# Kernel tuning notes

Hardware: AMD Instinct MI355X
Metric: run time of the kernel (lower is better)

Reference implementation:

```python
import jax, jax.numpy as jnp
import numpy as np


def setup_inputs() -> dict:
    key = jax.random.key(0)
    k1, k2 = jax.random.split(key)
    STATE_LEN, SEQ_LEN, HIDDEN = 8192, 8192, 1024
    out_state = jax.random.normal(k1, (STATE_LEN, HIDDEN), dtype=jnp.float32)
    history = jax.random.normal(k2, (SEQ_LEN, HIDDEN), dtype=jnp.float32)
    return {"out_state": out_state, "history": history}


def reference(out_state, history):
    # attn_energies[i, j] = dot(out_state[i], history[j])  ->  single GEMM
    energies = jnp.einsum('ih,jh->ij', out_state, history)  # [state_len, seq_len]
    # legacy F.softmax on a 2D tensor normalizes along dim=1 (the seq_len axis)
    return jax.nn.softmax(energies, axis=-1)
```

## Files before the change

### kernel.cpp

```cpp
#include <hip/hip_runtime.h>
#include <hip/hip_bf16.h>

#define M 8192
#define N 8192
#define K 1024
#define BM 128
#define BN 128
#define BK 64
#define ARR (BM*BK)

typedef __attribute__((ext_vector_type(8))) short short8;
typedef __attribute__((ext_vector_type(4))) float f32x4;

__device__ inline short f2bf(float x){
    __hip_bfloat16 h = __float2bfloat16(x);
    short s; __builtin_memcpy(&s, &h, 2); return s;
}
__device__ inline float bf2f(short s){
    __hip_bfloat16 h; __builtin_memcpy(&h, &s, 2);
    return __bfloat162float(h);
}

__device__ inline void conv8(float4 x0, float4 x1, short8& hi, short8& lo){
    float xs[8] = {x0.x,x0.y,x0.z,x0.w,x1.x,x1.y,x1.z,x1.w};
    #pragma unroll
    for (int j=0;j<8;++j){
        short h = f2bf(xs[j]);
        float r = xs[j] - bf2f(h);
        hi[j] = h; lo[j] = f2bf(r);
    }
}

__global__ __launch_bounds__(256) void presplit(
    const float* __restrict__ A, const float* __restrict__ B,
    short* __restrict__ Ah, short* __restrict__ Al,
    short* __restrict__ Bh, short* __restrict__ Bl)
{
    size_t c = (size_t)blockIdx.x * 256 + threadIdx.x;
    const float* src; short *dh, *dl; size_t off;
    const size_t perMat = (size_t)M * K / 8;
    if (c < perMat){ src = A; dh = Ah; dl = Al; off = c * 8; }
    else           { src = B; dh = Bh; dl = Bl; off = (c - perMat) * 8; }
    float4 x0 = *(const float4*)(src + off);
    float4 x1 = *(const float4*)(src + off + 4);
    short8 hi, lo;
    conv8(x0, x1, hi, lo);
    *(short8*)(dh + off) = hi;
    *(short8*)(dl + off) = lo;
}

#define GLOAD_LDS16(gp, lp) \
    __builtin_amdgcn_global_load_lds((const __attribute__((address_space(1))) void*)(gp), \
                                     (__attribute__((address_space(3))) void*)(lp), 16, 0, 0)

__global__ __launch_bounds__(512, 2)
void gemm_db(const short* __restrict__ Ahg, const short* __restrict__ Alg,
             const short* __restrict__ Bhg, const short* __restrict__ Blg,
             float* __restrict__ C)
{
    __shared__ __align__(16) short lds[2][4][ARR];

    const int tid  = threadIdx.x;
    const int lane = tid & 63, wid = tid >> 6;

    const int hw  = blockIdx.x;
    const int xcd = hw & 7;
    const int ix  = hw >> 3;
    const int gst = xcd * 32 + (ix >> 4);
    const int pos = ix & 15;
    const int bm0 = ((gst >> 4) * 4 + (pos >> 2)) * BM;
    const int bn0 = ((gst & 15) * 4 + (pos & 3)) * BN;

    const int wr = wid >> 2, wc = wid & 3;
    const int fr = lane & 15, fg = lane >> 4;

    f32x4 acc[4][2] = {};

    auto STAGE = [&](int buf, int kt){
        #pragma unroll
        for (int i = 0; i < 2; ++i){
            int bs = wid * 128 + i * 64;
            int s  = bs + lane;
            int row = s >> 3, sp = s & 7;
            int col8 = sp ^ (row & 7);
            size_t ga = (size_t)(bm0 + row) * K + kt * BK + col8 * 8;
            size_t gb = (size_t)(bn0 + row) * K + kt * BK + col8 * 8;
            GLOAD_LDS16(Ahg + ga, &lds[buf][0][bs * 8]);
            GLOAD_LDS16(Alg + ga, &lds[buf][1][bs * 8]);
            GLOAD_LDS16(Bhg + gb, &lds[buf][2][bs * 8]);
            GLOAD_LDS16(Blg + gb, &lds[buf][3][bs * 8]);
        }
    };

    STAGE(0, 0);
    __syncthreads();
    int cur = 0;

    for (int kt = 0; kt < K/BK; ++kt){
        if (kt + 1 < K/BK) STAGE(cur ^ 1, kt + 1);

        const short* sAh = lds[cur][0];
        const short* sAl = lds[cur][1];
        const short* sBh = lds[cur][2];
        const short* sBl = lds[cur][3];

        #pragma unroll
        for (int ks = 0; ks < 2; ++ks){
            short8 ah[4], al[4], bh[2], bl[2];
            #pragma unroll
            for (int m = 0; m < 4; ++m){
                int row = wr * 64 + m * 16 + fr;
                int idx = row * BK + ((((ks << 2) | fg) ^ (row & 7)) << 3);
                ah[m] = *(const short8*)&sAh[idx];
                al[m] = *(const short8*)&sAl[idx];
            }
            #pragma unroll
            for (int n = 0; n < 2; ++n){
                int row = wc * 32 + n * 16 + fr;
                int idx = row * BK + ((((ks << 2) | fg) ^ (row & 7)) << 3);
                bh[n] = *(const short8*)&sBh[idx];
                bl[n] = *(const short8*)&sBl[idx];
            }
            __builtin_amdgcn_s_setprio(1);
            #pragma unroll
            for (int m = 0; m < 4; ++m){
                #pragma unroll
                for (int n = 0; n < 2; ++n){
                    acc[m][n] = __builtin_amdgcn_mfma_f32_16x16x32_bf16(ah[m], bh[n], acc[m][n], 0, 0, 0);
                    acc[m][n] = __builtin_amdgcn_mfma_f32_16x16x32_bf16(ah[m], bl[n], acc[m][n], 0, 0, 0);
                    acc[m][n] = __builtin_amdgcn_mfma_f32_16x16x32_bf16(al[m], bh[n], acc[m][n], 0, 0, 0);
                }
            }
            __builtin_amdgcn_s_setprio(0);
        }
        __syncthreads();
        cur ^= 1;
    }

    #pragma unroll
    for (int m = 0; m < 4; ++m){
        int grow = bm0 + wr * 64 + m * 16 + fg * 4;
        #pragma unroll
        for (int r = 0; r < 4; ++r){
            float* crow = C + (size_t)(grow + r) * N + bn0 + wc * 32 + fr;
            crow[0]  = acc[m][0][r];
            crow[16] = acc[m][1][r];
        }
    }
}

__global__ __launch_bounds__(256, 2)
void gemm_fb(const float* __restrict__ A, const float* __restrict__ B,
             float* __restrict__ C)
{
    __shared__ __align__(16) short sAh[ARR];
    __shared__ __align__(16) short sAl[ARR];
    __shared__ __align__(16) short sBh[ARR];
    __shared__ __align__(16) short sBl[ARR];

    const int tid  = threadIdx.x;
    const int lane = tid & 63, wid = tid >> 6;
    const int bm0 = blockIdx.y * BM, bn0 = blockIdx.x * BN;
    const int wr = wid >> 1, wc = wid & 1;
    const int fr = lane & 15, fg = lane >> 4;

    f32x4 acc[4][4] = {};

    for (int kt = 0; kt < K/BK; ++kt){
        #pragma unroll
        for (int i = 0; i < 4; ++i){
            int s = tid + i * 256;
            int row = s >> 3, sp = s & 7;
            int widx = row * BK + ((sp ^ (row & 7)) << 3);
            const float* ga = A + (size_t)(bm0 + row) * K + kt * BK + sp * 8;
            float4 a0 = *(const float4*)ga, a1 = *(const float4*)(ga + 4);
            short8 hi, lo;
            conv8(a0, a1, hi, lo);
            *(short8*)&sAh[widx] = hi;
            *(short8*)&sAl[widx] = lo;
            const float* gb = B + (size_t)(bn0 + row) * K + kt * BK + sp * 8;
            float4 b0 = *(const float4*)gb, b1 = *(const float4*)(gb + 4);
            conv8(b0, b1, hi, lo);
            *(short8*)&sBh[widx] = hi;
            *(short8*)&sBl[widx] = lo;
        }
        __syncthreads();

        #pragma unroll
        for (int ks = 0; ks < 2; ++ks){
            short8 ah[4], al[4], bh[4], bl[4];
            #pragma unroll
            for (int m = 0; m < 4; ++m){
                int row = wr * 64 + m * 16 + fr;
                int idx = row * BK + ((((ks << 2) | fg) ^ (row & 7)) << 3);
                ah[m] = *(const short8*)&sAh[idx];
                al[m] = *(const short8*)&sAl[idx];
            }
            #pragma unroll
            for (int n = 0; n < 4; ++n){
                int row = wc * 64 + n * 16 + fr;
                int idx = row * BK + ((((ks << 2) | fg) ^ (row & 7)) << 3);
                bh[n] = *(const short8*)&sBh[idx];
                bl[n] = *(const short8*)&sBl[idx];
            }
            #pragma unroll
            for (int m = 0; m < 4; ++m){
                #pragma unroll
                for (int n = 0; n < 4; ++n){
                    acc[m][n] = __builtin_amdgcn_mfma_f32_16x16x32_bf16(ah[m], bh[n], acc[m][n], 0, 0, 0);
                    acc[m][n] = __builtin_amdgcn_mfma_f32_16x16x32_bf16(ah[m], bl[n], acc[m][n], 0, 0, 0);
                    acc[m][n] = __builtin_amdgcn_mfma_f32_16x16x32_bf16(al[m], bh[n], acc[m][n], 0, 0, 0);
                }
            }
        }
        __syncthreads();
    }

    #pragma unroll
    for (int m = 0; m < 4; ++m){
        int grow = bm0 + wr * 64 + m * 16 + fg * 4;
        #pragma unroll
        for (int r = 0; r < 4; ++r){
            float* crow = C + (size_t)(grow + r) * N + bn0 + wc * 64 + fr;
            #pragma unroll
            for (int n = 0; n < 4; ++n)
                crow[n * 16] = acc[m][n][r];
        }
    }
}

__global__ __launch_bounds__(256) void softmax_fused(float* __restrict__ E)
{
    const int row = blockIdx.x;
    const int tid = threadIdx.x;
    const int lane = tid & 63, wid = tid >> 6;
    float4* rp = (float4*)(E + (size_t)row * N);
    float4 v[8];
    float mx = -3.4e38f;
    #pragma unroll
    for (int i = 0; i < 8; ++i){
        v[i] = rp[tid + i * 256];
        mx = fmaxf(mx, fmaxf(fmaxf(v[i].x, v[i].y), fmaxf(v[i].z, v[i].w)));
    }
    #pragma unroll
    for (int off = 32; off; off >>= 1) mx = fmaxf(mx, __shfl_xor(mx, off));
    __shared__ float redm[4], reds[4];
    if (lane == 0) redm[wid] = mx;
    __syncthreads();
    mx = fmaxf(fmaxf(redm[0], redm[1]), fmaxf(redm[2], redm[3]));
    float s = 0.f;
    #pragma unroll
    for (int i = 0; i < 8; ++i){
        v[i].x = __expf(v[i].x - mx); v[i].y = __expf(v[i].y - mx);
        v[i].z = __expf(v[i].z - mx); v[i].w = __expf(v[i].w - mx);
        s += v[i].x + v[i].y + v[i].z + v[i].w;
    }
    #pragma unroll
    for (int off = 32; off; off >>= 1) s += __shfl_xor(s, off);
    if (lane == 0) reds[wid] = s;
    __syncthreads();
    float inv = 1.0f / (reds[0] + reds[1] + reds[2] + reds[3]);
    #pragma unroll
    for (int i = 0; i < 8; ++i){
        float4 o = v[i];
        o.x *= inv; o.y *= inv; o.z *= inv; o.w *= inv;
        rp[tid + i * 256] = o;
    }
}

extern "C" void kernel_launch(void* const* d_in, const int* in_sizes, int n_in,
                              void* d_out, int out_size, void* d_ws, size_t ws_size,
                              hipStream_t stream)
{
    const float* A = (const float*)d_in[0];
    const float* B = (const float*)d_in[1];
    float* out = (float*)d_out;

    const size_t elems = (size_t)M * K;
    const size_t splitBytes = 4 * elems * sizeof(short);

    if (ws_size >= splitBytes){
        short* Ah = (short*)d_ws;
        short* Al = Ah + elems;
        short* Bh = Al + elems;
        short* Bl = Bh + elems;
        presplit<<<8192, 256, 0, stream>>>(A, B, Ah, Al, Bh, Bl);
        gemm_db<<<(M/BM)*(N/BN), 512, 0, stream>>>(Ah, Al, Bh, Bl, out);
    } else {
        gemm_fb<<<dim3(N/BN, M/BM), 256, 0, stream>>>(A, B, out);
    }
    softmax_fused<<<M, 256, 0, stream>>>(out);
}
```

Measured before the change: 466.3 us.

## Use 256x256 tiles with k-major presplit layout for contiguous LDS loads

The presplit kernel now writes the bf16 hi/lo splits in a k8-major layout, so each 8-element k chunk for consecutive rows is contiguous. The GEMM tile grows from 128x128 to 256x256 with BK=32, and each wave owns an 8x4 grid of MFMA fragments. Each wave loads one array slice straight into LDS without swizzling, and the XCD-aware block remap is simplified. The aim is more data reuse per LDS load and lower global traffic. The cost is much higher register pressure (128 accumulator floats per lane plus fragments), which may reduce occupancy or spill under launch_bounds(512,2), and possible LDS bank conflicts from the unswizzled reads.

```diff
diff --git a/kernel.cpp b/kernel.cpp
--- a/kernel.cpp
+++ b/kernel.cpp
@@ -4,10 +4,10 @@
 #define M 8192
 #define N 8192
 #define K 1024
-#define BM 128
-#define BN 128
-#define BK 64
-#define ARR (BM*BK)
+#define BM 256
+#define BN 256
+#define BK 32
+#define KT (K/BK)
 
 typedef __attribute__((ext_vector_type(8))) short short8;
 typedef __attribute__((ext_vector_type(4))) float f32x4;
@@ -31,64 +31,63 @@
     }
 }
 
-__global__ __launch_bounds__(256) void presplit(
-    const float* __restrict__ A, const float* __restrict__ B,
-    short* __restrict__ Ah, short* __restrict__ Al,
-    short* __restrict__ Bh, short* __restrict__ Bl)
-{
-    size_t c = (size_t)blockIdx.x * 256 + threadIdx.x;
-    const float* src; short *dh, *dl; size_t off;
-    const size_t perMat = (size_t)M * K / 8;
-    if (c < perMat){ src = A; dh = Ah; dl = Al; off = c * 8; }
-    else           { src = B; dh = Bh; dl = Bl; off = (c - perMat) * 8; }
-    float4 x0 = *(const float4*)(src + off);
-    float4 x1 = *(const float4*)(src + off + 4);
-    short8 hi, lo;
-    conv8(x0, x1, hi, lo);
-    *(short8*)(dh + off) = hi;
-    *(short8*)(dl + off) = lo;
-}
-
 #define GLOAD_LDS16(gp, lp) \
     __builtin_amdgcn_global_load_lds((const __attribute__((address_space(1))) void*)(gp), \
                                      (__attribute__((address_space(3))) void*)(lp), 16, 0, 0)
 
+__global__ __launch_bounds__(512) void presplit_t(
+    const float* __restrict__ A, const float* __restrict__ B,
+    short* __restrict__ Aht, short* __restrict__ Alt,
+    short* __restrict__ Bht, short* __restrict__ Blt)
+{
+    size_t c = (size_t)blockIdx.x * 512 + threadIdx.x;
+    const float* src; short *dh, *dl;
+    const size_t perMat = (size_t)M * (K/8);
+    if (c < perMat){ src = A; dh = Aht; dl = Alt; }
+    else { c -= perMat; src = B; dh = Bht; dl = Blt; }
+    int row = (int)(c >> 7);
+    int k8  = (int)(c & 127);
+    const float* p = src + (size_t)row * K + k8 * 8;
+    float4 x0 = *(const float4*)p;
+    float4 x1 = *(const float4*)(p + 4);
+    short8 hi, lo; conv8(x0, x1, hi, lo);
+    size_t o = ((size_t)k8 * M + row) * 8;
+    *(short8*)(dh + o) = hi;
+    *(short8*)(dl + o) = lo;
+}
+
 __global__ __launch_bounds__(512, 2)
-void gemm_db(const short* __restrict__ Ahg, const short* __restrict__ Alg,
-             const short* __restrict__ Bhg, const short* __restrict__ Blg,
-             float* __restrict__ C)
-{
-    __shared__ __align__(16) short lds[2][4][ARR];
+void gemm_t(const short* __restrict__ Aht, const short* __restrict__ Alt,
+            const short* __restrict__ Bht, const short* __restrict__ Blt,
+            float* __restrict__ C)
+{
+    __shared__ __align__(16) short lds[2][4][4][BM][8];
 
     const int tid  = threadIdx.x;
     const int lane = tid & 63, wid = tid >> 6;
 
-    const int hw  = blockIdx.x;
-    const int xcd = hw & 7;
-    const int ix  = hw >> 3;
-    const int gst = xcd * 32 + (ix >> 4);
-    const int pos = ix & 15;
-    const int bm0 = ((gst >> 4) * 4 + (pos >> 2)) * BM;
-    const int bn0 = ((gst & 15) * 4 + (pos & 3)) * BN;
+    const int xcd = blockIdx.x & 7;
+    const int gid = xcd * 128 + (blockIdx.x >> 3);
+    const int bm0 = (gid >> 5) * BM;
+    const int bn0 = (gid & 31) * BN;
 
     const int wr = wid >> 2, wc = wid & 3;
     const int fr = lane & 15, fg = lane >> 4;
 
-    f32x4 acc[4][2] = {};
+    const int arr = wid >> 1;
+    const short* gp = (arr == 0) ? Aht : (arr == 1) ? Alt : (arr == 2) ? Bht : Blt;
+    const int   gb  = (arr < 2) ? bm0 : bn0;
+    const int sbase = (wid & 1) * 2;
+
+    f32x4 acc[8][4] = {};
 
     auto STAGE = [&](int buf, int kt){
         #pragma unroll
-        for (int i = 0; i < 2; ++i){
-            int bs = wid * 128 + i * 64;
-            int s  = bs + lane;
-            int row = s >> 3, sp = s & 7;
-            int col8 = sp ^ (row & 7);
-            size_t ga = (size_t)(bm0 + row) * K + kt * BK + col8 * 8;
-            size_t gb = (size_t)(bn0 + row) * K + kt * BK + col8 * 8;
-            GLOAD_LDS16(Ahg + ga, &lds[buf][0][bs * 8]);
-            GLOAD_LDS16(Alg + ga, &lds[buf][1][bs * 8]);
-            GLOAD_LDS16(Bhg + gb, &lds[buf][2][bs * 8]);
-            GLOAD_LDS16(Blg + gb, &lds[buf][3][bs * 8]);
+        for (int i = 0; i < 8; ++i){
+            int s  = sbase + (i >> 2);
+            int rb = i & 3;
+            const short* src = gp + (((size_t)(kt * 4 + s)) * M + gb + rb * 64 + lane) * 8;
+            GLOAD_LDS16(src, &lds[buf][arr][s][rb * 64][0]);
         }
     };
 
@@ -96,90 +95,87 @@
     __syncthreads();
     int cur = 0;
 
-    for (int kt = 0; kt < K/BK; ++kt){
-        if (kt + 1 < K/BK) STAGE(cur ^ 1, kt + 1);
-
-        const short* sAh = lds[cur][0];
-        const short* sAl = lds[cur][1];
-        const short* sBh = lds[cur][2];
-        const short* sBl = lds[cur][3];
-
-        #pragma unroll
-        for (int ks = 0; ks < 2; ++ks){
-            short8 ah[4], al[4], bh[2], bl[2];
-            #pragma unroll
-            for (int m = 0; m < 4; ++m){
-                int row = wr * 64 + m * 16 + fr;
-                int idx = row * BK + ((((ks << 2) | fg) ^ (row & 7)) << 3);
-                ah[m] = *(const short8*)&sAh[idx];
-                al[m] = *(const short8*)&sAl[idx];
-            }
-            #pragma unroll
-            for (int n = 0; n < 2; ++n){
-                int row = wc * 32 + n * 16 + fr;
-                int idx = row * BK + ((((ks << 2) | fg) ^ (row & 7)) << 3);
-                bh[n] = *(const short8*)&sBh[idx];
-                bl[n] = *(const short8*)&sBl[idx];
-            }
-            __builtin_amdgcn_s_setprio(1);
-            #pragma unroll
-            for (int m = 0; m < 4; ++m){
-                #pragma unroll
-                for (int n = 0; n < 2; ++n){
-                    acc[m][n] = __builtin_amdgcn_mfma_f32_16x16x32_bf16(ah[m], bh[n], acc[m][n], 0, 0, 0);
-                    acc[m][n] = __builtin_amdgcn_mfma_f32_16x16x32_bf16(ah[m], bl[n], acc[m][n], 0, 0, 0);
-                    acc[m][n] = __builtin_amdgcn_mfma_f32_16x16x32_bf16(al[m], bh[n], acc[m][n], 0, 0, 0);
-                }
-            }
-            __builtin_amdgcn_s_setprio(0);
-        }
+    for (int kt = 0; kt < KT; ++kt){
+        if (kt + 1 < KT) STAGE(cur ^ 1, kt + 1);
+
+        short8 ah[8], al[8], bh[4], bl[4];
+        #pragma unroll
+        for (int m = 0; m < 8; ++m){
+            int row = wr * 128 + m * 16 + fr;
+            ah[m] = *(const short8*)&lds[cur][0][fg][row][0];
+            al[m] = *(const short8*)&lds[cur][1][fg][row][0];
+        }
+        #pragma unroll
+        for (int n = 0; n < 4; ++n){
+            int row = wc * 64 + n * 16 + fr;
+            bh[n] = *(const short8*)&lds[cur][2][fg][row][0];
+            bl[n] = *(const short8*)&lds[cur][3][fg][row][0];
+        }
+
+        __builtin_amdgcn_s_setprio(1);
+        #pragma unroll
+        for (int m = 0; m < 8; ++m){
+            #pragma unroll
+            for (int n = 0; n < 4; ++n){
+                acc[m][n] = __builtin_amdgcn_mfma_f32_16x16x32_bf16(ah[m], bh[n], acc[m][n], 0, 0, 0);
+                acc[m][n] = __builtin_amdgcn_mfma_f32_16x16x32_bf16(ah[m], bl[n], acc[m][n], 0, 0, 0);
+                acc[m][n] = __builtin_amdgcn_mfma_f32_16x16x32_bf16(al[m], bh[n], acc[m][n], 0, 0, 0);
+            }
+        }
+        __builtin_amdgcn_s_setprio(0);
+
         __syncthreads();
         cur ^= 1;
     }
 
     #pragma unroll
-    for (int m = 0; m < 4; ++m){
-        int grow = bm0 + wr * 64 + m * 16 + fg * 4;
+    for (int m = 0; m < 8; ++m){
+        int grow = bm0 + wr * 128 + m * 16 + fg * 4;
         #pragma unroll
         for (int r = 0; r < 4; ++r){
-            float* crow = C + (size_t)(grow + r) * N + bn0 + wc * 32 + fr;
-            crow[0]  = acc[m][0][r];
-            crow[16] = acc[m][1][r];
-        }
-    }
-}
-
+            float* crow = C + (size_t)(grow + r) * N + bn0 + wc * 64 + fr;
+            #pragma unroll
+            for (int n = 0; n < 4; ++n)
+                crow[n * 16] = acc[m][n][r];
+        }
+    }
+}
+
+#define FBM 128
+#define FBN 128
+#define FBK 64
+#define FARR (FBM*FBK)
 __global__ __launch_bounds__(256, 2)
 void gemm_fb(const float* __restrict__ A, const float* __restrict__ B,
              float* __restrict__ C)
 {
-    __shared__ __align__(16) short sAh[ARR];
-    __shared__ __align__(16) short sAl[ARR];
-    __shared__ __align__(16) short sBh[ARR];
-    __shared__ __align__(16) short sBl[ARR];
+    __shared__ __align__(16) short sAh[FARR];
+    __shared__ __align__(16) short sAl[FARR];
+    __shared__ __align__(16) short sBh[FARR];
+    __shared__ __align__(16) short sBl[FARR];
 
     const int tid  = threadIdx.x;
     const int lane = tid & 63, wid = tid >> 6;
-    const int bm0 = blockIdx.y * BM, bn0 = blockIdx.x * BN;
+    const int bm0 = blockIdx.y * FBM, bn0 = blockIdx.x * FBN;
     const int wr = wid >> 1, wc = wid & 1;
     const int fr = lane & 15, fg = lane >> 4;
 
     f32x4 acc[4][4] = {};
 
-    for (int kt = 0; kt < K/BK; ++kt){
+    for (int kt = 0; kt < K/FBK; ++kt){
         #pragma unroll
         for (int i = 0; i < 4; ++i){
             int s = tid + i * 256;
             int row = s >> 3, sp = s & 7;
-            int widx = row * BK + ((sp ^ (row & 7)) << 3);
-            const float* ga = A + (size_t)(bm0 + row) * K + kt * BK + sp * 8;
+            int widx = row * FBK + ((sp ^ (row & 7)) << 3);
+            const float* ga = A + (size_t)(bm0 + row) * K + kt * FBK + sp * 8;
             float4 a0 = *(const float4*)ga, a1 = *(const float4*)(ga + 4);
             short8 hi, lo;
             conv8(a0, a1, hi, lo);
             *(short8*)&sAh[widx] = hi;
             *(short8*)&sAl[widx] = lo;
-            const float* gb = B + (size_t)(bn0 + row) * K + kt * BK + sp * 8;
-            float4 b0 = *(const float4*)gb, b1 = *(const float4*)(gb + 4);
+            const float* gbp = B + (size_t)(bn0 + row) * K + kt * FBK + sp * 8;
+            float4 b0 = *(const float4*)gbp, b1 = *(const float4*)(gbp + 4);
             conv8(b0, b1, hi, lo);
             *(short8*)&sBh[widx] = hi;
             *(short8*)&sBl[widx] = lo;
@@ -192,14 +188,14 @@
             #pragma unroll
             for (int m = 0; m < 4; ++m){
                 int row = wr * 64 + m * 16 + fr;
-                int idx = row * BK + ((((ks << 2) | fg) ^ (row & 7)) << 3);
+                int idx = row * FBK + ((((ks << 2) | fg) ^ (row & 7)) << 3);
                 ah[m] = *(const short8*)&sAh[idx];
                 al[m] = *(const short8*)&sAl[idx];
             }
             #pragma unroll
             for (int n = 0; n < 4; ++n){
                 int row = wc * 64 + n * 16 + fr;
-                int idx = row * BK + ((((ks << 2) | fg) ^ (row & 7)) << 3);
+                int idx = row * FBK + ((((ks << 2) | fg) ^ (row & 7)) << 3);
                 bh[n] = *(const short8*)&sBh[idx];
                 bl[n] = *(const short8*)&sBl[idx];
             }
@@ -280,14 +276,14 @@
     const size_t splitBytes = 4 * elems * sizeof(short);
 
     if (ws_size >= splitBytes){
-        short* Ah = (short*)d_ws;
-        short* Al = Ah + elems;
-        short* Bh = Al + elems;
-        short* Bl = Bh + elems;
-        presplit<<<8192, 256, 0, stream>>>(A, B, Ah, Al, Bh, Bl);
-        gemm_db<<<(M/BM)*(N/BN), 512, 0, stream>>>(Ah, Al, Bh, Bl, out);
+        short* Aht = (short*)d_ws;
+        short* Alt = Aht + elems;
+        short* Bht = Alt + elems;
+        short* Blt = Bht + elems;
+        presplit_t<<<4096, 512, 0, stream>>>(A, B, Aht, Alt, Bht, Blt);
+        gemm_t<<<(M/BM)*(N/BN), 512, 0, stream>>>(Aht, Alt, Bht, Blt, out);
     } else {
-        gemm_fb<<<dim3(N/BN, M/BM), 256, 0, stream>>>(A, B, out);
+        gemm_fb<<<dim3(N/FBN, M/FBM), 256, 0, stream>>>(A, B, out);
     }
     softmax_fused<<<M, 256, 0, stream>>>(out);
 }
```

Result: faster. 453.8 us (-2.7%).
